# Kernel tuning notes

Hardware: AMD Instinct MI355X
Metric: run time of the kernel (lower is better)

## Reference

```python
import jax, jax.numpy as jnp
import numpy as np

B, S, D = 2, 2048, 1024
H = 16
HD = D // H   # 64
K = 64        # local_window / neighbors per position


def setup_inputs() -> dict:
    key = jax.random.key(0)
    k1, k2, k3, k4, k5, k6 = jax.random.split(key, 6)
    scale = 1.0 / np.sqrt(D)
    x = jax.random.normal(k1, (B, S, D), dtype=jnp.float32)
    routes = jax.random.randint(k2, (S, K), 0, S, dtype=jnp.int64)
    W_qkv = jax.random.normal(k3, (D, 3 * D), dtype=jnp.float32) * scale
    b_qkv = jnp.zeros((3 * D,), dtype=jnp.float32)
    W_proj = jax.random.normal(k4, (D, D), dtype=jnp.float32) * scale
    b_proj = jnp.zeros((D,), dtype=jnp.float32)
    return {"x": x, "W_qkv": W_qkv, "b_qkv": b_qkv,
            "W_proj": W_proj, "b_proj": b_proj, "routes": routes}


def reference(x, W_qkv, b_qkv, W_proj, b_proj, routes):
    # x: (B, S, D)
    qkv = x @ W_qkv + b_qkv                       # (B, S, 3D)
    qkv = qkv.reshape(B, S, 3, H, HD)
    q, k, v = qkv[:, :, 0], qkv[:, :, 1], qkv[:, :, 2]   # (B, S, H, HD)
    q = q.transpose(0, 2, 1, 3)                   # (B, H, S, HD)
    k = k.transpose(0, 2, 1, 3)
    v = v.transpose(0, 2, 1, 3)

    r = jnp.clip(routes, 0, S - 1)                # (S, K)
    # Gather neighbor keys/values: (B, H, S, K, HD)
    k_n = k[:, :, r, :]
    v_n = v[:, :, r, :]

    scores = jnp.einsum('bhsd,bhskd->bhsk', q, k_n) / jnp.sqrt(
        jnp.asarray(HD, dtype=q.dtype))           # (B, H, S, K)
    attn = jax.nn.softmax(scores, axis=-1)
    out = jnp.einsum('bhsk,bhskd->bhsd', attn, v_n)       # (B, H, S, HD)

    out = out.transpose(0, 2, 1, 3).reshape(B, S, D)
    return out @ W_proj + b_proj
```

## Files before the change

### kernel.cpp

```cpp
#include <hip/hip_runtime.h>
#include <stdint.h>

#define B_ 2
#define S_ 2048
#define D_ 1024
#define H_ 16
#define HD_ 64
#define K_ 64

typedef __attribute__((ext_vector_type(8))) __bf16 bf16x8v;
typedef __attribute__((ext_vector_type(4))) float f32x4;
typedef __attribute__((ext_vector_type(8))) unsigned short ushort8v;

#define GLD_LDS16(g, l)                                                        \
  __builtin_amdgcn_global_load_lds(                                            \
      (const __attribute__((address_space(1))) void*)(g),                      \
      (__attribute__((address_space(3))) void*)(l), 16, 0, 0)

__device__ __forceinline__ float bf2f(unsigned short u) {
  union { unsigned u32; float f; } c;
  c.u32 = ((unsigned)u) << 16;
  return c.f;
}
__device__ __forceinline__ unsigned short f2bf(float f) {
  union { float f; unsigned u; } c;
  c.f = f;
  unsigned u = c.u;
  u += 0x7fffu + ((u >> 16) & 1u);
  return (unsigned short)(u >> 16);
}

__global__ __launch_bounds__(256) void prep_fused(
    const float* __restrict__ x, unsigned short* __restrict__ x_bf,
    const float* __restrict__ Wqkv, unsigned short* __restrict__ wqkvT,
    const float* __restrict__ Wproj, unsigned short* __restrict__ wprojT) {
  __shared__ float tile[64][65];
  const int bid = blockIdx.x;
  const int t = threadIdx.x;

  if (bid < 4096) {
    const int i = bid * 256 + t;
    float4 v = ((const float4*)x)[i];
    ushort4 o;
    o.x = f2bf(v.x); o.y = f2bf(v.y); o.z = f2bf(v.z); o.w = f2bf(v.w);
    ((ushort4*)x_bf)[i] = o;
    return;
  }

  const float* W;
  unsigned short* WT;
  int R, C, bx, by;
  if (bid < 4096 + 768) {
    const int b2 = bid - 4096;
    W = Wqkv; WT = wqkvT; R = D_; C = 3 * D_;
    by = b2 / 48; bx = b2 - by * 48;
  } else {
    const int b3 = bid - 4096 - 768;
    W = Wproj; WT = wprojT; R = D_; C = D_;
    by = b3 >> 4; bx = b3 & 15;
  }
  const int r0 = by * 64;
  const int c0 = bx * 64;
#pragma unroll
  for (int i = 0; i < 16; ++i) {
    int idx = t + i * 256;
    int rr = idx >> 6, cc = idx & 63;
    tile[rr][cc] = W[(size_t)(r0 + rr) * C + c0 + cc];
  }
  __syncthreads();
#pragma unroll
  for (int i = 0; i < 16; ++i) {
    int idx = t + i * 256;
    int rr = idx >> 6, cc = idx & 63;
    WT[(size_t)(c0 + rr) * R + r0 + cc] = f2bf(tile[cc][rr]);
  }
}

template <bool OUT_F32>
__global__ __launch_bounds__(256) void gemm_bias(
    const unsigned short* __restrict__ A, const unsigned short* __restrict__ Bt,
    const float* __restrict__ bias, void* __restrict__ Cout,
    int M, int N, int Kd) {
  __shared__ unsigned short As[128 * 32];
  __shared__ unsigned short Bs[128 * 32];
  const int t = threadIdx.x;
  const int w = t >> 6;
  const int l = t & 63;
  const int m0 = blockIdx.y * 128;
  const int n0 = blockIdx.x * 128;
  const int wr = w >> 1, wc = w & 1;

  f32x4 acc[4][4] = {};

  const int srow = t >> 2;
  const int scol = (t & 3) * 8;
  char* asBase = (char*)As + w * 1024;
  char* bsBase = (char*)Bs + w * 1024;

  const int lr = l & 15;
  const int kh = (l >> 4) * 8;

  const int KT = Kd >> 5;
  for (int kt = 0; kt < KT; ++kt) {
    const int k0 = kt << 5;
    {
      const unsigned short* g0 = A + (size_t)(m0 + srow) * Kd + k0 + scol;
      const unsigned short* g1 = A + (size_t)(m0 + 64 + srow) * Kd + k0 + scol;
      GLD_LDS16(g0, asBase);
      GLD_LDS16(g1, asBase + 4096);
      const unsigned short* h0 = Bt + (size_t)(n0 + srow) * Kd + k0 + scol;
      const unsigned short* h1 = Bt + (size_t)(n0 + 64 + srow) * Kd + k0 + scol;
      GLD_LDS16(h0, bsBase);
      GLD_LDS16(h1, bsBase + 4096);
    }
    __syncthreads();
    bf16x8v af[4], bfv[4];
#pragma unroll
    for (int m = 0; m < 4; ++m)
      af[m] = *(const bf16x8v*)&As[(wr * 64 + m * 16 + lr) * 32 + kh];
#pragma unroll
    for (int n = 0; n < 4; ++n)
      bfv[n] = *(const bf16x8v*)&Bs[(wc * 64 + n * 16 + lr) * 32 + kh];
#pragma unroll
    for (int m = 0; m < 4; ++m)
#pragma unroll
      for (int n = 0; n < 4; ++n)
        acc[m][n] = __builtin_amdgcn_mfma_f32_16x16x32_bf16(af[m], bfv[n],
                                                            acc[m][n], 0, 0, 0);
    __syncthreads();
  }

  const int rbase = (l >> 4) * 4;
#pragma unroll
  for (int m = 0; m < 4; ++m) {
#pragma unroll
    for (int n = 0; n < 4; ++n) {
      const int gc = n0 + wc * 64 + n * 16 + lr;
      const float bv = bias[gc];
#pragma unroll
      for (int j = 0; j < 4; ++j) {
        const int gr = m0 + wr * 64 + m * 16 + rbase + j;
        float v = acc[m][n][j] + bv;
        if (OUT_F32)
          ((float*)Cout)[(size_t)gr * N + gc] = v;
        else
          ((unsigned short*)Cout)[(size_t)gr * N + gc] = f2bf(v);
      }
    }
  }
}

__global__ __launch_bounds__(256) void attn_kernel(
    const unsigned short* __restrict__ qkv, const int* __restrict__ routes,
    unsigned short* __restrict__ outp) {
  __shared__ float sc[16][68];
  __shared__ unsigned rtsoff[64];
  __shared__ float pbuf[1024];
  const int bs = blockIdx.x;
  const int b = bs >> 11;
  const int s = bs & (S_ - 1);
  const int t = threadIdx.x;
  const int w = t >> 6, l = t & 63;
  const int kh2 = w >> 1, hh = w & 1;

  if (t < 64) {
    int r = routes[s * K_ + t];
    r = min(max(r, 0), S_ - 1);
    rtsoff[t] = (unsigned)(b * S_ + r) * 3072u;
  }
  __syncthreads();

  const unsigned colo = hh * 512 + l * 8;
  const int head = colo >> 6;
  const size_t rowbase = (size_t)bs * 3072;

  float q[8];
  {
    ushort8v u = *(const ushort8v*)(qkv + rowbase + colo);
#pragma unroll
    for (int i = 0; i < 8; ++i) q[i] = bf2f(u[i]) * 0.125f;
  }

  const unsigned kofs = 1024u + colo;
  const unsigned vofs = 2048u + colo;
  const int jbase = kh2 * 32;

#pragma unroll 4
  for (int j2 = 0; j2 < 32; ++j2) {
    const int j = jbase + j2;
    ushort8v u = *(const ushort8v*)(qkv + (rtsoff[j] + kofs));
    float d = q[0] * bf2f(u[0]);
#pragma unroll
    for (int i = 1; i < 8; ++i) d += q[i] * bf2f(u[i]);
    d += __shfl_xor(d, 1);
    d += __shfl_xor(d, 2);
    d += __shfl_xor(d, 4);
    if ((l & 7) == 0) sc[head][j] = d;
  }
  __syncthreads();

  {
    const int h = t >> 4;
    const int l2 = t & 15;
    float v0 = sc[h][l2], v1 = sc[h][l2 + 16], v2 = sc[h][l2 + 32],
          v3 = sc[h][l2 + 48];
    float m = fmaxf(fmaxf(v0, v1), fmaxf(v2, v3));
    m = fmaxf(m, __shfl_xor(m, 1));
    m = fmaxf(m, __shfl_xor(m, 2));
    m = fmaxf(m, __shfl_xor(m, 4));
    m = fmaxf(m, __shfl_xor(m, 8));
    v0 = __expf(v0 - m); v1 = __expf(v1 - m);
    v2 = __expf(v2 - m); v3 = __expf(v3 - m);
    float ss = v0 + v1 + v2 + v3;
    ss += __shfl_xor(ss, 1);
    ss += __shfl_xor(ss, 2);
    ss += __shfl_xor(ss, 4);
    ss += __shfl_xor(ss, 8);
    float inv = 1.0f / ss;
    sc[h][l2] = v0 * inv;
    sc[h][l2 + 16] = v1 * inv;
    sc[h][l2 + 32] = v2 * inv;
    sc[h][l2 + 48] = v3 * inv;
  }
  __syncthreads();

  float acc[8] = {};
#pragma unroll 4
  for (int j2 = 0; j2 < 32; ++j2) {
    const int j = jbase + j2;
    ushort8v u = *(const ushort8v*)(qkv + (rtsoff[j] + vofs));
    const float p = sc[head][j];
#pragma unroll
    for (int i = 0; i < 8; ++i) acc[i] += p * bf2f(u[i]);
  }

  if (kh2 == 1) {
    f32x4 a0 = {acc[0], acc[1], acc[2], acc[3]};
    f32x4 a1 = {acc[4], acc[5], acc[6], acc[7]};
    *(f32x4*)&pbuf[colo] = a0;
    *(f32x4*)&pbuf[colo + 4] = a1;
  }
  __syncthreads();
  if (kh2 == 0) {
    ushort8v o;
#pragma unroll
    for (int i = 0; i < 8; ++i) o[i] = f2bf(acc[i] + pbuf[colo + i]);
    *(ushort8v*)(outp + (size_t)bs * D_ + colo) = o;
  }
}

extern "C" void kernel_launch(void* const* d_in, const int* in_sizes, int n_in,
                              void* d_out, int out_size, void* d_ws,
                              size_t ws_size, hipStream_t stream) {
  const float* x = (const float*)d_in[0];
  const float* Wqkv = (const float*)d_in[1];
  const float* bqkv = (const float*)d_in[2];
  const float* Wproj = (const float*)d_in[3];
  const float* bproj = (const float*)d_in[4];
  const int* routes = (const int*)d_in[5];
  float* out = (float*)d_out;

  char* ws = (char*)d_ws;
  unsigned short* x_bf = (unsigned short*)(ws);
  unsigned short* wqkvT = (unsigned short*)(ws + 8388608);
  unsigned short* wprojT = (unsigned short*)(ws + 14680064);
  unsigned short* qkv = (unsigned short*)(ws + 16777216);
  unsigned short* aout = (unsigned short*)(ws + 41943040);

  prep_fused<<<5120, 256, 0, stream>>>(x, x_bf, Wqkv, wqkvT, Wproj, wprojT);

  gemm_bias<false><<<dim3(3 * D_ / 128, B_ * S_ / 128), 256, 0, stream>>>(
      x_bf, wqkvT, bqkv, qkv, B_ * S_, 3 * D_, D_);
  attn_kernel<<<B_ * S_, 256, 0, stream>>>(qkv, routes, aout);
  gemm_bias<true><<<dim3(D_ / 128, B_ * S_ / 128), 256, 0, stream>>>(
      aout, wprojT, bproj, out, B_ * S_, D_, D_);
}
```

Before: 143.2 us.

## Double GEMM K-tile to 64 with XOR-swizzled LDS layout

The GEMM now stages a 64-wide K slice per iteration instead of 32, which halves the number of barrier pairs and loop iterations. The LDS layout is XOR-swizzled by row to avoid bank conflicts on the wider 128-byte rows. Each iteration issues twice the MFMAs per sync. This doubles LDS usage and register pressure from fragment arrays, and there is still no double buffering.

```diff
diff --git a/kernel.cpp b/kernel.cpp
--- a/kernel.cpp
+++ b/kernel.cpp
@@ -81,8 +81,8 @@
     const unsigned short* __restrict__ A, const unsigned short* __restrict__ Bt,
     const float* __restrict__ bias, void* __restrict__ Cout,
     int M, int N, int Kd) {
-  __shared__ unsigned short As[128 * 32];
-  __shared__ unsigned short Bs[128 * 32];
+  __shared__ unsigned short As[128 * 64];
+  __shared__ unsigned short Bs[128 * 64];
   const int t = threadIdx.x;
   const int w = t >> 6;
   const int l = t & 63;
@@ -92,41 +92,52 @@
 
   f32x4 acc[4][4] = {};
 
-  const int srow = t >> 2;
-  const int scol = (t & 3) * 8;
+  const int g_r = t >> 3;
+  const int scol = ((t & 7) * 8) ^ ((g_r & 7) * 8);
   char* asBase = (char*)As + w * 1024;
   char* bsBase = (char*)Bs + w * 1024;
 
   const int lr = l & 15;
-  const int kh = (l >> 4) * 8;
-
-  const int KT = Kd >> 5;
+  const int kq = (l >> 4) * 8;
+  const int xr = (lr & 7) * 8;
+
+  const int KT = Kd >> 6;
   for (int kt = 0; kt < KT; ++kt) {
-    const int k0 = kt << 5;
+    const int k0 = kt << 6;
     {
-      const unsigned short* g0 = A + (size_t)(m0 + srow) * Kd + k0 + scol;
-      const unsigned short* g1 = A + (size_t)(m0 + 64 + srow) * Kd + k0 + scol;
-      GLD_LDS16(g0, asBase);
-      GLD_LDS16(g1, asBase + 4096);
-      const unsigned short* h0 = Bt + (size_t)(n0 + srow) * Kd + k0 + scol;
-      const unsigned short* h1 = Bt + (size_t)(n0 + 64 + srow) * Kd + k0 + scol;
-      GLD_LDS16(h0, bsBase);
-      GLD_LDS16(h1, bsBase + 4096);
+#pragma unroll
+      for (int i = 0; i < 4; ++i)
+        GLD_LDS16(A + (size_t)(m0 + i * 32 + g_r) * Kd + k0 + scol,
+                  asBase + i * 4096);
+#pragma unroll
+      for (int i = 0; i < 4; ++i)
+        GLD_LDS16(Bt + (size_t)(n0 + i * 32 + g_r) * Kd + k0 + scol,
+                  bsBase + i * 4096);
     }
     __syncthreads();
-    bf16x8v af[4], bfv[4];
+    bf16x8v af[4][2], bfv[4][2];
+#pragma unroll
+    for (int m = 0; m < 4; ++m) {
+      const int row = wr * 64 + m * 16 + lr;
+#pragma unroll
+      for (int ks = 0; ks < 2; ++ks)
+        af[m][ks] = *(const bf16x8v*)&As[row * 64 + ((ks * 32 + kq) ^ xr)];
+    }
+#pragma unroll
+    for (int n = 0; n < 4; ++n) {
+      const int row = wc * 64 + n * 16 + lr;
+#pragma unroll
+      for (int ks = 0; ks < 2; ++ks)
+        bfv[n][ks] = *(const bf16x8v*)&Bs[row * 64 + ((ks * 32 + kq) ^ xr)];
+    }
 #pragma unroll
     for (int m = 0; m < 4; ++m)
-      af[m] = *(const bf16x8v*)&As[(wr * 64 + m * 16 + lr) * 32 + kh];
-#pragma unroll
-    for (int n = 0; n < 4; ++n)
-      bfv[n] = *(const bf16x8v*)&Bs[(wc * 64 + n * 16 + lr) * 32 + kh];
-#pragma unroll
-    for (int m = 0; m < 4; ++m)
 #pragma unroll
       for (int n = 0; n < 4; ++n)
-        acc[m][n] = __builtin_amdgcn_mfma_f32_16x16x32_bf16(af[m], bfv[n],
-                                                            acc[m][n], 0, 0, 0);
+#pragma unroll
+        for (int ks = 0; ks < 2; ++ks)
+          acc[m][n] = __builtin_amdgcn_mfma_f32_16x16x32_bf16(
+              af[m][ks], bfv[n][ks], acc[m][n], 0, 0, 0);
     __syncthreads();
   }
 
```

After: 136.0 us. -5.0%, faster.

## Double-buffer GEMM LDS tiles and XOR-swizzle K columns to cut bank conflicts

Applied to the files above, without the earlier changes.

The bf16 MFMA GEMM now keeps two LDS buffers for A and B. The global-to-LDS load for the next K tile is issued before the MFMAs on the current tile run, so each iteration needs one barrier instead of two and global latency can overlap compute. It also XOR-swizzles the 8-element column slot by row index, applied on the global load side and undone on the LDS read side, to reduce LDS bank conflicts on the fragment reads. This doubles the GEMM's LDS use, which may lower occupancy, and it depends on the barrier waiting for the asynchronous LDS loads to finish.

```diff
diff --git a/kernel.cpp b/kernel.cpp
--- a/kernel.cpp
+++ b/kernel.cpp
@@ -81,8 +81,8 @@
     const unsigned short* __restrict__ A, const unsigned short* __restrict__ Bt,
     const float* __restrict__ bias, void* __restrict__ Cout,
     int M, int N, int Kd) {
-  __shared__ unsigned short As[128 * 32];
-  __shared__ unsigned short Bs[128 * 32];
+  __shared__ unsigned short As[2][128 * 32];
+  __shared__ unsigned short Bs[2][128 * 32];
   const int t = threadIdx.x;
   const int w = t >> 6;
   const int l = t & 63;
@@ -93,42 +93,51 @@
   f32x4 acc[4][4] = {};
 
   const int srow = t >> 2;
-  const int scol = (t & 3) * 8;
-  char* asBase = (char*)As + w * 1024;
-  char* bsBase = (char*)Bs + w * 1024;
+  const int scol = ((t & 3) * 8) ^ ((srow & 3) * 8);
+  const int wofs = w * 1024;
 
   const int lr = l & 15;
-  const int kh = (l >> 4) * 8;
+  const int kq = (l >> 4) * 8;
+  const int kqs = kq ^ ((lr & 3) * 8);
+
+#define STAGE_AB(kt, buf)                                                      \
+  {                                                                            \
+    GLD_LDS16(A + (size_t)(m0 + srow) * Kd + (kt) * 32 + scol,                 \
+              (char*)&As[buf][0] + wofs);                                      \
+    GLD_LDS16(A + (size_t)(m0 + 64 + srow) * Kd + (kt) * 32 + scol,            \
+              (char*)&As[buf][0] + wofs + 4096);                               \
+    GLD_LDS16(Bt + (size_t)(n0 + srow) * Kd + (kt) * 32 + scol,                \
+              (char*)&Bs[buf][0] + wofs);                                      \
+    GLD_LDS16(Bt + (size_t)(n0 + 64 + srow) * Kd + (kt) * 32 + scol,           \
+              (char*)&Bs[buf][0] + wofs + 4096);                               \
+  }
 
   const int KT = Kd >> 5;
+  STAGE_AB(0, 0);
+  __syncthreads();
+
+  int cur = 0;
   for (int kt = 0; kt < KT; ++kt) {
-    const int k0 = kt << 5;
-    {
-      const unsigned short* g0 = A + (size_t)(m0 + srow) * Kd + k0 + scol;
-      const unsigned short* g1 = A + (size_t)(m0 + 64 + srow) * Kd + k0 + scol;
-      GLD_LDS16(g0, asBase);
-      GLD_LDS16(g1, asBase + 4096);
-      const unsigned short* h0 = Bt + (size_t)(n0 + srow) * Kd + k0 + scol;
-      const unsigned short* h1 = Bt + (size_t)(n0 + 64 + srow) * Kd + k0 + scol;
-      GLD_LDS16(h0, bsBase);
-      GLD_LDS16(h1, bsBase + 4096);
-    }
-    __syncthreads();
+    if (kt + 1 < KT) STAGE_AB(kt + 1, cur ^ 1);
+
     bf16x8v af[4], bfv[4];
 #pragma unroll
     for (int m = 0; m < 4; ++m)
-      af[m] = *(const bf16x8v*)&As[(wr * 64 + m * 16 + lr) * 32 + kh];
+      af[m] = *(const bf16x8v*)&As[cur][(wr * 64 + m * 16 + lr) * 32 + kqs];
 #pragma unroll
     for (int n = 0; n < 4; ++n)
-      bfv[n] = *(const bf16x8v*)&Bs[(wc * 64 + n * 16 + lr) * 32 + kh];
+      bfv[n] = *(const bf16x8v*)&Bs[cur][(wc * 64 + n * 16 + lr) * 32 + kqs];
 #pragma unroll
     for (int m = 0; m < 4; ++m)
 #pragma unroll
       for (int n = 0; n < 4; ++n)
         acc[m][n] = __builtin_amdgcn_mfma_f32_16x16x32_bf16(af[m], bfv[n],
                                                             acc[m][n], 0, 0, 0);
+
     __syncthreads();
-  }
+    cur ^= 1;
+  }
+#undef STAGE_AB
 
   const int rbase = (l >> 4) * 4;
 #pragma unroll
```

New measurement: 136.9 us. 1.05x faster.
